# Kernel tuning notes

Measured on AMD Instinct MI355X. Metric: run time of the kernel, lower is better.

Reference implementation:

```python
import jax, jax.numpy as jnp
import numpy as np

N_NODES = 100000
N_EDGES = 1600000
N_GRAPHS = 512
IN_CH = 64
HID = 128
LAT = 64
MAX_NODES = 128
OUT_SIZE = MAX_NODES * (MAX_NODES - 1) // 2  # 8128


def _gcn_conv(x, W, b, src, dst, n):
    """PyG GCNConv: x' = D^-1/2 (A+I) D^-1/2 (x W) + b, degrees include self-loops."""
    h = x @ W  # [N, out]
    deg = jnp.zeros((n,), h.dtype).at[dst].add(1.0) + 1.0  # in-degree + self-loop
    dinv = jax.lax.rsqrt(deg)
    norm = dinv[src] * dinv[dst]  # [E]
    agg = jnp.zeros_like(h).at[dst].add(h[src] * norm[:, None])  # neighbor scatter-add
    agg = agg + h * (dinv * dinv)[:, None]  # self-loop term, norm = 1/deg
    return agg + b


def setup_inputs() -> dict:
    key = jax.random.key(0)
    ks = jax.random.split(key, 20)
    s = 0.02
    inp = {
        "x": jax.random.normal(ks[0], (N_NODES, IN_CH), jnp.float32),
        "edge_index": jax.random.randint(ks[1], (2, N_EDGES), 0, N_NODES),
        "batch": jnp.sort(jax.random.randint(ks[2], (N_NODES,), 0, N_GRAPHS)),
        "eps": jax.random.normal(ks[3], (N_GRAPHS, LAT), jnp.float32),
        # encoder params
        "W1": jax.random.normal(ks[4], (IN_CH, HID), jnp.float32) * s,
        "b1": jnp.zeros((HID,), jnp.float32),
        "W2": jax.random.normal(ks[5], (HID, HID), jnp.float32) * s,
        "b2": jnp.zeros((HID,), jnp.float32),
        "Wmu": jax.random.normal(ks[6], (HID, LAT), jnp.float32) * s,
        "bmu": jnp.zeros((LAT,), jnp.float32),
        "Wlv": jax.random.normal(ks[7], (HID, LAT), jnp.float32) * s,
        "blv": jnp.zeros((LAT,), jnp.float32),
        # decoder MLP params
        "D1": jax.random.normal(ks[8], (LAT, HID), jnp.float32) * s,
        "d1": jnp.zeros((HID,), jnp.float32),
        "D2": jax.random.normal(ks[9], (HID, HID), jnp.float32) * s,
        "d2": jnp.zeros((HID,), jnp.float32),
        "D3": jax.random.normal(ks[10], (HID, OUT_SIZE), jnp.float32) * s,
        "d3": jnp.zeros((OUT_SIZE,), jnp.float32),
    }
    return inp


def reference(x, edge_index, batch, eps, W1, b1, W2, b2, Wmu, bmu, Wlv, blv,
              D1, d1, D2, d2, D3, d3):
    src, dst = edge_index[0], edge_index[1]
    # --- encoder: two GCN layers + ReLU ---
    h = jax.nn.relu(_gcn_conv(x, W1, b1, src, dst, N_NODES))
    h = jax.nn.relu(_gcn_conv(h, W2, b2, src, dst, N_NODES))
    # --- global mean pool by graph id ---
    sums = jax.ops.segment_sum(h, batch, num_segments=N_GRAPHS)
    cnts = jax.ops.segment_sum(jnp.ones((N_NODES,), h.dtype), batch, num_segments=N_GRAPHS)
    h_graph = sums / jnp.maximum(cnts, 1.0)[:, None]  # [G, HID]
    mu = h_graph @ Wmu + bmu
    logvar = h_graph @ Wlv + blv
    # --- reparameterise ---
    z = mu + eps * jnp.exp(0.5 * logvar)  # [G, LAT]
    # --- MLP decoder -> symmetric adjacency ---
    p = jax.nn.relu(z @ D1 + d1)
    p = jax.nn.relu(p @ D2 + d2)
    probs = jax.nn.sigmoid(p @ D3 + d3)  # [G, OUT_SIZE]
    r, c = jnp.triu_indices(MAX_NODES, k=1)
    adj = jnp.zeros((N_GRAPHS, MAX_NODES, MAX_NODES), probs.dtype)
    adj = adj.at[:, r, c].set(probs)
    adj = adj + jnp.swapaxes(adj, 1, 2)
    return adj, mu, logvar
```

## Files before the change

### kernel.cpp

```cpp
#include <hip/hip_runtime.h>
#include <hip/hip_fp16.h>

#define NN 100000
#define NE 1600000
#define NG 512
#define OUTS 8128
#define NB2 196
#define CHUNK 8192
#define NPB 196

typedef short bf16x8 __attribute__((ext_vector_type(8)));
typedef _Float16 f16x8 __attribute__((ext_vector_type(8)));
typedef _Float16 f16x2 __attribute__((ext_vector_type(2)));
typedef float f32x4 __attribute__((ext_vector_type(4)));

__device__ __forceinline__ unsigned pack_bf16x2(float a, float b) {
    unsigned ua = __float_as_uint(a);
    unsigned ub = __float_as_uint(b);
    ua = (ua + 0x7fffu + ((ua >> 16) & 1u)) >> 16;
    ub = (ub + 0x7fffu + ((ub >> 16) & 1u)) >> 16;
    return ua | (ub << 16);
}
__device__ __forceinline__ unsigned short f2bf(float f) {
    unsigned u = __float_as_uint(f);
    u = (u + 0x7fffu + ((u >> 16) & 1u)) >> 16;
    return (unsigned short)u;
}
__device__ __forceinline__ unsigned cvt_pkrtz_u(float a, float b) {
    auto h = __builtin_amdgcn_cvt_pkrtz(a, b);
    union { decltype(h) h2; unsigned u; } c; c.h2 = h; return c.u;
}
__device__ __forceinline__ f16x2 u2h(unsigned u) { union { unsigned u; f16x2 h; } c; c.u = u; return c.h; }

__device__ __forceinline__ unsigned f2fp8(float f) {
    unsigned h = (unsigned)__half_as_ushort(__float2half(f * 0.00390625f));
    return (h + 0x3Fu + ((h >> 7) & 1u)) >> 7;
}
__device__ __forceinline__ unsigned f2fp8s(float f) {
    unsigned h = (unsigned)__half_as_ushort(__float2half(f * 0.00390625f));
    unsigned s = (h >> 8) & 0x80u;
    unsigned mag = h & 0x7fffu;
    return s | ((mag + 0x3Fu + ((mag >> 7) & 1u)) >> 7);
}

#define DECO(W, LO, HI) { LO += u2h(((W) & 0x007f007fu) << 7); HI += u2h(((W) & 0x7f007f00u) >> 1); }
#define DECOS(W, LO, HI) { \
    LO += u2h((((W) & 0x007f007fu) << 7) | (((W) & 0x00800080u) << 8)); \
    HI += u2h((((W) & 0x7f007f00u) >> 1) | ((W) & 0x80008000u)); }

__global__ __launch_bounds__(512) void k_part(const int* __restrict__ src, const int* __restrict__ dst,
        int* __restrict__ tmp, int* __restrict__ scanhist) {
    __shared__ int hist[NB2], cur[NB2], scan[256];
    int p = blockIdx.x, t = threadIdx.x;
    int e0 = p * CHUNK;
    int e1 = min(e0 + CHUNK, NE);
    for (int i = t; i < NB2; i += 512) hist[i] = 0;
    __syncthreads();
    for (int e = e0 + t; e < e1; e += 512)
        atomicAdd(&hist[dst[e] >> 9], 1);
    __syncthreads();
    int h = 0;
    if (t < 256) { h = (t < NB2) ? hist[t] : 0; scan[t] = h; }
    __syncthreads();
    for (int off = 1; off < 256; off <<= 1) {
        int v = (t < 256 && t >= off) ? scan[t - off] : 0;
        __syncthreads();
        if (t < 256) scan[t] += v;
        __syncthreads();
    }
    if (t < NB2) {
        int excl = scan[t] - h;
        cur[t] = excl;
        scanhist[p * (NB2 + 1) + t] = excl;
    }
    if (t == 0) scanhist[p * (NB2 + 1) + NB2] = e1 - e0;
    __syncthreads();
    for (int e = e0 + t; e < e1; e += 512) {
        int d = dst[e];
        int b = d >> 9;
        int r = atomicAdd(&cur[b], 1);
        tmp[e0 + r] = (src[e] << 9) | (d & 511);
    }
}

__global__ __launch_bounds__(256) void k_btotseg(const int* __restrict__ scanhist,
        int* __restrict__ bucketbase, const int* __restrict__ batch, int* __restrict__ seg_end) {
    if (blockIdx.x == 0) {
        __shared__ int sc[256];
        int b = threadIdx.x;
        int tot = 0;
        if (b < NB2) {
            for (int p = 0; p < NPB; ++p)
                tot += scanhist[p * (NB2 + 1) + b + 1] - scanhist[p * (NB2 + 1) + b];
        }
        sc[b] = tot;
        __syncthreads();
        for (int off = 1; off < 256; off <<= 1) {
            int v = (b >= off) ? sc[b - off] : 0;
            __syncthreads();
            sc[b] += v;
            __syncthreads();
        }
        if (b < NB2) bucketbase[b] = sc[b] - tot;
    } else {
        int i = (blockIdx.x - 1) * 256 + threadIdx.x;
        if (i >= NN) return;
        int b = batch[i];
        int bn = (i == NN - 1) ? NG : batch[i + 1];
        for (int g = b; g < bn; ++g) seg_end[g] = i + 1;
        if (i == 0) {
            for (int g = 0; g < b; ++g) seg_end[g] = 0;
        }
    }
}

__global__ __launch_bounds__(1024) void k_fill2(const int* __restrict__ bucketbase,
        const int* __restrict__ scanhist, const int* __restrict__ tmp,
        int* __restrict__ colidx, int* __restrict__ cnti, int* __restrict__ rowptr,
        float* __restrict__ dinv, const float* __restrict__ x, unsigned* __restrict__ u1b) {
    __shared__ int lc[512], rb[512], sc[256];
    __shared__ float ldv[512];
    int b = blockIdx.x, t = threadIdx.x;
    int n0 = b << 9;
    if (t < 512) lc[t] = 0;
    __syncthreads();
    int w = t >> 6, lane = t & 63;
    for (int p = w; p < NPB; p += 16) {
        int s0 = scanhist[p * (NB2 + 1) + b];
        int s1 = scanhist[p * (NB2 + 1) + b + 1];
        int base = p * CHUNK;
        for (int i = s0 + lane; i < s1; i += 64)
            atomicAdd(&lc[tmp[base + i] & 511], 1);
    }
    __syncthreads();
    int v0 = 0, v1 = 0, s = 0;
    if (t < 256) { v0 = lc[2 * t]; v1 = lc[2 * t + 1]; s = v0 + v1; sc[t] = s; }
    __syncthreads();
    for (int off = 1; off < 256; off <<= 1) {
        int xv = (t < 256 && t >= off) ? sc[t - off] : 0;
        __syncthreads();
        if (t < 256) sc[t] += xv;
        __syncthreads();
    }
    if (t < 256) {
        int excl = sc[t] - s;
        int base0 = bucketbase[b];
        rb[2 * t] = base0 + excl;
        rb[2 * t + 1] = base0 + excl + v0;
        float dv0 = rsqrtf((float)v0 + 1.0f);
        float dv1 = rsqrtf((float)v1 + 1.0f);
        ldv[2 * t] = dv0;
        ldv[2 * t + 1] = dv1;
        int node0 = n0 + 2 * t;
        if (node0 < NN) {
            cnti[node0] = v0;
            rowptr[node0] = base0 + excl;
            dinv[node0] = dv0;
        }
        if (node0 + 1 < NN) {
            cnti[node0 + 1] = v1;
            rowptr[node0 + 1] = base0 + excl + v0;
            dinv[node0 + 1] = dv1;
        }
    }
    __syncthreads();
    if (t < 512) lc[t] = 0;
    __syncthreads();
    for (int p = w; p < NPB; p += 16) {
        int s0 = scanhist[p * (NB2 + 1) + b];
        int s1 = scanhist[p * (NB2 + 1) + b + 1];
        int base = p * CHUNK;
        for (int i = s0 + lane; i < s1; i += 64) {
            int v = tmp[base + i];
            int dl = v & 511;
            int pos = atomicAdd(&lc[dl], 1);
            colidx[rb[dl] + pos] = v >> 9;
        }
    }
    for (int i = t; i < 512 * 16; i += 1024) {
        int local = i >> 4, c = i & 15;
        int node = n0 + local;
        if (node >= NN) continue;
        float4 xv = *(const float4*)&x[(long)node * 64 + c * 4];
        float d = ldv[local];
        unsigned o = f2fp8s(xv.x * d) | (f2fp8s(xv.y * d) << 8)
                   | (f2fp8s(xv.z * d) << 16) | (f2fp8s(xv.w * d) << 24);
        u1b[node * 16 + c] = o;
    }
}

__global__ __launch_bounds__(256) void k_wtall(const float* __restrict__ W1,
        const float* __restrict__ W2, const float* __restrict__ D3,
        unsigned short* __restrict__ wt1, unsigned short* __restrict__ wt2,
        unsigned short* __restrict__ wt3t) {
    __shared__ float tile[32][33];
    int blk = blockIdx.x;
    if (blk < 96) {
        int i = blk * 256 + threadIdx.x;
        if (i < 8192) {
            int n = i >> 6, k = i & 63;
            wt1[i] = (unsigned short)__half_as_ushort(__float2half(W1[k * 128 + n]));
        } else {
            int e = i - 8192;
            int n = e >> 7, k = e & 127;
            wt2[e] = f2bf(W2[k * 128 + n]);
        }
    } else {
        int bb = blk - 96;
        int n0 = (bb % 254) * 32, k0 = (bb / 254) * 32;
        for (int i = threadIdx.x; i < 1024; i += 256) {
            int kk = i >> 5, nn = i & 31;
            tile[kk][nn] = D3[(long)(k0 + kk) * OUTS + n0 + nn];
        }
        __syncthreads();
        for (int i = threadIdx.x; i < 1024; i += 256) {
            int nn = i >> 5, kk = i & 31;
            wt3t[(long)(n0 + nn) * 128 + k0 + kk] =
                (unsigned short)__half_as_ushort(__float2half(tile[kk][nn]));
        }
    }
}

__global__ __launch_bounds__(256) void k_gather1(const int* __restrict__ rowptr,
        const int* __restrict__ cnti, const int* __restrict__ colidx,
        const unsigned* __restrict__ u, const float* __restrict__ dinv,
        unsigned* __restrict__ s1) {
    int node = blockIdx.x * 64 + (threadIdx.x >> 2);
    if (node >= NN) return;
    int lane = threadIdx.x & 3;
    const uint4* uf = (const uint4*)u;
    uint4 self = uf[node * 4 + lane];
    f16x2 z = {(_Float16)0.f, (_Float16)0.f};
    f16x2 la0 = z, ha0 = z, la1 = z, ha1 = z, la2 = z, ha2 = z, la3 = z, ha3 = z;
    f16x2 lb0 = z, hb0 = z, lb1 = z, hb1 = z, lb2 = z, hb2 = z, lb3 = z, hb3 = z;
    DECOS(self.x, la0, ha0) DECOS(self.y, la1, ha1) DECOS(self.z, la2, ha2) DECOS(self.w, la3, ha3)
    int n = cnti[node];
    const int* ci = colidx + rowptr[node];
    int j = 0;
    for (; j + 4 <= n; j += 4) {
        uint4 va = uf[ci[j] * 4 + lane];
        uint4 vb = uf[ci[j + 1] * 4 + lane];
        uint4 vc = uf[ci[j + 2] * 4 + lane];
        uint4 vd = uf[ci[j + 3] * 4 + lane];
        DECOS(va.x, la0, ha0) DECOS(va.y, la1, ha1) DECOS(va.z, la2, ha2) DECOS(va.w, la3, ha3)
        DECOS(vb.x, lb0, hb0) DECOS(vb.y, lb1, hb1) DECOS(vb.z, lb2, hb2) DECOS(vb.w, lb3, hb3)
        DECOS(vc.x, la0, ha0) DECOS(vc.y, la1, ha1) DECOS(vc.z, la2, ha2) DECOS(vc.w, la3, ha3)
        DECOS(vd.x, lb0, hb0) DECOS(vd.y, lb1, hb1) DECOS(vd.z, lb2, hb2) DECOS(vd.w, lb3, hb3)
    }
    for (; j < n; ++j) {
        uint4 va = uf[ci[j] * 4 + lane];
        DECOS(va.x, la0, ha0) DECOS(va.y, la1, ha1) DECOS(va.z, la2, ha2) DECOS(va.w, la3, ha3)
    }
    la0 += lb0; ha0 += hb0; la1 += lb1; ha1 += hb1;
    la2 += lb2; ha2 += hb2; la3 += lb3; ha3 += hb3;
    float d = dinv[node] * 256.0f;
    uint4 o1, o2;
    o1.x = cvt_pkrtz_u((float)la0[0] * d, (float)ha0[0] * d);
    o1.y = cvt_pkrtz_u((float)la0[1] * d, (float)ha0[1] * d);
    o1.z = cvt_pkrtz_u((float)la1[0] * d, (float)ha1[0] * d);
    o1.w = cvt_pkrtz_u((float)la1[1] * d, (float)ha1[1] * d);
    o2.x = cvt_pkrtz_u((float)la2[0] * d, (float)ha2[0] * d);
    o2.y = cvt_pkrtz_u((float)la2[1] * d, (float)ha2[1] * d);
    o2.z = cvt_pkrtz_u((float)la3[0] * d, (float)ha3[0] * d);
    o2.w = cvt_pkrtz_u((float)la3[1] * d, (float)ha3[1] * d);
    *(uint4*)&s1[node * 32 + lane * 8] = o1;
    *(uint4*)&s1[node * 32 + lane * 8 + 4] = o2;
}

__global__ __launch_bounds__(256) void k_gather2(const int* __restrict__ rowptr,
        const int* __restrict__ cnti, const int* __restrict__ colidx,
        const unsigned* __restrict__ u, const float* __restrict__ dinv,
        unsigned* __restrict__ s2) {
    int node = blockIdx.x * 32 + (threadIdx.x >> 3);
    int lane = threadIdx.x & 7;
    const uint4* uf = (const uint4*)u;
    uint4 self = uf[node * 8 + lane];
    f16x2 z = {(_Float16)0.f, (_Float16)0.f};
    f16x2 la0 = z, ha0 = z, la1 = z, ha1 = z, la2 = z, ha2 = z, la3 = z, ha3 = z;
    f16x2 lb0 = z, hb0 = z, lb1 = z, hb1 = z, lb2 = z, hb2 = z, lb3 = z, hb3 = z;
    DECO(self.x, la0, ha0) DECO(self.y, la1, ha1) DECO(self.z, la2, ha2) DECO(self.w, la3, ha3)
    int n = cnti[node];
    const int* ci = colidx + rowptr[node];
    int j = 0;
    for (; j + 4 <= n; j += 4) {
        uint4 va = uf[ci[j] * 8 + lane];
        uint4 vb = uf[ci[j + 1] * 8 + lane];
        uint4 vc = uf[ci[j + 2] * 8 + lane];
        uint4 vd = uf[ci[j + 3] * 8 + lane];
        DECO(va.x, la0, ha0) DECO(va.y, la1, ha1) DECO(va.z, la2, ha2) DECO(va.w, la3, ha3)
        DECO(vb.x, lb0, hb0) DECO(vb.y, lb1, hb1) DECO(vb.z, lb2, hb2) DECO(vb.w, lb3, hb3)
        DECO(vc.x, la0, ha0) DECO(vc.y, la1, ha1) DECO(vc.z, la2, ha2) DECO(vc.w, la3, ha3)
        DECO(vd.x, lb0, hb0) DECO(vd.y, lb1, hb1) DECO(vd.z, lb2, hb2) DECO(vd.w, lb3, hb3)
    }
    for (; j < n; ++j) {
        uint4 va = uf[ci[j] * 8 + lane];
        DECO(va.x, la0, ha0) DECO(va.y, la1, ha1) DECO(va.z, la2, ha2) DECO(va.w, la3, ha3)
    }
    la0 += lb0; ha0 += hb0; la1 += lb1; ha1 += hb1;
    la2 += lb2; ha2 += hb2; la3 += lb3; ha3 += hb3;
    float d = dinv[node] * 16.0f;
    uint4 o1, o2;
    o1.x = pack_bf16x2((float)la0[0] * d, (float)ha0[0] * d);
    o1.y = pack_bf16x2((float)la0[1] * d, (float)ha0[1] * d);
    o1.z = pack_bf16x2((float)la1[0] * d, (float)ha1[0] * d);
    o1.w = pack_bf16x2((float)la1[1] * d, (float)ha1[1] * d);
    o2.x = pack_bf16x2((float)la2[0] * d, (float)ha2[0] * d);
    o2.y = pack_bf16x2((float)la2[1] * d, (float)ha2[1] * d);
    o2.z = pack_bf16x2((float)la3[0] * d, (float)ha3[0] * d);
    o2.w = pack_bf16x2((float)la3[1] * d, (float)ha3[1] * d);
    *(uint4*)&s2[node * 64 + lane * 8] = o1;
    *(uint4*)&s2[node * 64 + lane * 8 + 4] = o2;
}

template<int K, int EPI, int AF16>
__global__ __launch_bounds__(256) void k_gemm_mfma(const unsigned short* __restrict__ Ab,
        const unsigned short* __restrict__ wt, const float* __restrict__ dinv,
        const float* __restrict__ bias, void* __restrict__ outp) {
    constexpr int KS = K / 32;
    constexpr int SLOTS = K / 8;
    __shared__ __align__(16) unsigned short wlds[128 * K];
    char* lb = (char*)wlds;
    for (int c = threadIdx.x; c < 128 * SLOTS; c += 256) {
        int n = c / SLOTS, s = c - n * SLOTS;
        *(uint4*)(lb + n * (2 * K) + ((s ^ (n & 7)) << 4)) = *(const uint4*)(wt + c * 8);
    }
    __syncthreads();
    int lane = threadIdx.x & 63;
    int w = threadIdx.x >> 6;
    int r0 = blockIdx.x * 64 + w * 16;
    int arow = r0 + (lane & 15);
    if (arow >= NN) arow = NN - 1;
    bf16x8 af[KS];
    #pragma unroll
    for (int ks = 0; ks < KS; ++ks)
        af[ks] = *(const bf16x8*)&Ab[(long)arow * K + ks * 32 + (lane >> 4) * 8];
    f32x4 acc[8];
    #pragma unroll
    for (int t = 0; t < 8; ++t) acc[t] = (f32x4){0.f, 0.f, 0.f, 0.f};
    #pragma unroll
    for (int ks = 0; ks < KS; ++ks) {
        #pragma unroll
        for (int t = 0; t < 8; ++t) {
            int n = t * 16 + (lane & 15);
            int slot = ks * 4 + (lane >> 4);
            bf16x8 braw = *(const bf16x8*)(lb + n * (2 * K) + ((slot ^ (n & 7)) << 4));
            if constexpr (AF16) {
                union { bf16x8 r; f16x8 h; } ca, cb;
                ca.r = af[ks]; cb.r = braw;
                acc[t] = __builtin_amdgcn_mfma_f32_16x16x32_f16(ca.h, cb.h, acc[t], 0, 0, 0);
            } else {
                acc[t] = __builtin_amdgcn_mfma_f32_16x16x32_bf16(af[ks], braw, acc[t], 0, 0, 0);
            }
        }
    }
    float bv[8];
    #pragma unroll
    for (int t = 0; t < 8; ++t) bv[t] = bias[t * 16 + (lane & 15)];
    #pragma unroll
    for (int r = 0; r < 4; ++r) {
        long row = r0 + (lane >> 4) * 4 + r;
        if (row >= NN) continue;
        float d = dinv[row];
        #pragma unroll
        for (int t = 0; t < 8; ++t) {
            float val = fmaxf(acc[t][r] + bv[t], 0.f);
            int col = t * 16 + (lane & 15);
            if (EPI == 0)
                ((unsigned char*)outp)[row * 128 + col] = (unsigned char)f2fp8(val * (16.0f * d));
            else
                ((unsigned short*)outp)[row * 128 + col] = f2bf(val);
        }
    }
}

__global__ __launch_bounds__(256) void k_pooldec(const unsigned* __restrict__ h,
        const int* __restrict__ seg_end,
        const float* __restrict__ Wmu, const float* __restrict__ bmu,
        const float* __restrict__ Wlv, const float* __restrict__ blv,
        const float* __restrict__ eps,
        const float* __restrict__ D1, const float* __restrict__ d1,
        const float* __restrict__ D2, const float* __restrict__ d2,
        float* __restrict__ mu_o, float* __restrict__ lv_o,
        unsigned short* __restrict__ p2out) {
    __shared__ float part[3][128];
    __shared__ float row[128], mlv[128], zr[64], p1[128];
    int g = blockIdx.x;
    int w = threadIdx.x >> 6, t64 = threadIdx.x & 63;
    int s = (g == 0) ? 0 : seg_end[g - 1];
    int e = seg_end[g];
    float a0 = 0.f, a1 = 0.f;
    for (int i = s + w; i < e; i += 4) {
        unsigned u = h[(long)i * 64 + t64];
        a0 += __uint_as_float(u << 16);
        a1 += __uint_as_float(u & 0xffff0000u);
    }
    if (w) { part[w - 1][t64 * 2] = a0; part[w - 1][t64 * 2 + 1] = a1; }
    __syncthreads();
    if (w == 0) {
        a0 += part[0][t64 * 2] + part[1][t64 * 2] + part[2][t64 * 2];
        a1 += part[0][t64 * 2 + 1] + part[1][t64 * 2 + 1] + part[2][t64 * 2 + 1];
        float inv = (e > s) ? 1.0f / (float)(e - s) : 0.f;
        row[t64 * 2] = a0 * inv;
        row[t64 * 2 + 1] = a1 * inv;
    }
    __syncthreads();
    int t = threadIdx.x;
    if (t < 64) {
        float acc = bmu[t];
        for (int k = 0; k < 128; ++k) acc += row[k] * Wmu[k * 64 + t];
        mlv[t] = acc;
    } else if (t < 128) {
        int t2 = t - 64;
        float acc = blv[t2];
        for (int k = 0; k < 128; ++k) acc += row[k] * Wlv[k * 64 + t2];
        mlv[64 + t2] = acc;
    }
    __syncthreads();
    if (t < 64) {
        float mu = mlv[t], lv = mlv[64 + t];
        mu_o[g * 64 + t] = mu;
        lv_o[g * 64 + t] = lv;
        zr[t] = mu + eps[g * 64 + t] * expf(0.5f * lv);
    }
    __syncthreads();
    if (t < 128) {
        float acc = d1[t];
        for (int k = 0; k < 64; ++k) acc += zr[k] * D1[k * 128 + t];
        p1[t] = fmaxf(acc, 0.f);
    }
    __syncthreads();
    if (t < 128) {
        float acc = d2[t];
        for (int k = 0; k < 128; ++k) acc += p1[k] * D2[k * 128 + t];
        p2out[g * 128 + t] = (unsigned short)__half_as_ushort(__float2half(fmaxf(acc, 0.f)));
    }
}

__global__ __launch_bounds__(256) void k_dec3m(const unsigned short* __restrict__ Ab,
        const unsigned short* __restrict__ Wt, const float* __restrict__ b,
        float* __restrict__ out) {
    int lane = threadIdx.x & 63;
    int w = threadIdx.x >> 6;
    int r0 = blockIdx.x * 64 + w * 16;
    int c0 = blockIdx.y * 64;
    int arow = r0 + (lane & 15);
    f16x8 af[4];
    #pragma unroll
    for (int ks = 0; ks < 4; ++ks) {
        union { bf16x8 r; f16x8 h; } ca;
        ca.r = *(const bf16x8*)&Ab[arow * 128 + ks * 32 + (lane >> 4) * 8];
        af[ks] = ca.h;
    }
    f32x4 acc[4];
    #pragma unroll
    for (int nt = 0; nt < 4; ++nt) acc[nt] = (f32x4){0.f, 0.f, 0.f, 0.f};
    #pragma unroll
    for (int nt = 0; nt < 4; ++nt) {
        long n = c0 + nt * 16 + (lane & 15);
        #pragma unroll
        for (int ks = 0; ks < 4; ++ks) {
            union { bf16x8 r; f16x8 h; } cb;
            cb.r = *(const bf16x8*)&Wt[n * 128 + ks * 32 + (lane >> 4) * 8];
            acc[nt] = __builtin_amdgcn_mfma_f32_16x16x32_f16(af[ks], cb.h, acc[nt], 0, 0, 0);
        }
    }
    #pragma unroll
    for (int nt = 0; nt < 4; ++nt) {
        int col = c0 + nt * 16 + (lane & 15);
        float bias = b[col];
        #pragma unroll
        for (int r = 0; r < 4; ++r) {
            int row = r0 + (lane >> 4) * 4 + r;
            float v = acc[nt][r] + bias;
            out[(long)row * OUTS + col] = 1.f / (1.f + expf(-v));
        }
    }
}

__global__ __launch_bounds__(256) void k_adj(const float* __restrict__ probs, float* __restrict__ adj) {
    int t = blockIdx.x * 256 + threadIdx.x;
    int g = t >> 12;
    int rem = t & 4095;
    int r = rem >> 5;
    int c0 = (rem & 31) * 4;
    const float* pg = &probs[g * OUTS];
    float4 o;
    float* op = (float*)&o;
    #pragma unroll
    for (int j = 0; j < 4; ++j) {
        int c = c0 + j;
        if (c == r) { op[j] = 0.f; continue; }
        int a = c < r ? c : r;
        int b = c < r ? r : c;
        int k = a * (255 - a) / 2 + (b - a - 1);
        op[j] = pg[k];
    }
    *(float4*)&adj[(long)t * 4] = o;
}

extern "C" void kernel_launch(void* const* d_in, const int* in_sizes, int n_in,
                              void* d_out, int out_size, void* d_ws, size_t ws_size,
                              hipStream_t stream) {
    const float* x   = (const float*)d_in[0];
    const int*   ei  = (const int*)d_in[1];
    const int* batch = (const int*)d_in[2];
    const float* eps = (const float*)d_in[3];
    const float* W1  = (const float*)d_in[4];
    const float* b1  = (const float*)d_in[5];
    const float* W2  = (const float*)d_in[6];
    const float* b2  = (const float*)d_in[7];
    const float* Wmu = (const float*)d_in[8];
    const float* bmu = (const float*)d_in[9];
    const float* Wlv = (const float*)d_in[10];
    const float* blv = (const float*)d_in[11];
    const float* D1  = (const float*)d_in[12];
    const float* d1  = (const float*)d_in[13];
    const float* D2  = (const float*)d_in[14];
    const float* d2  = (const float*)d_in[15];
    const float* D3  = (const float*)d_in[16];
    const float* d3  = (const float*)d_in[17];

    const int* esrc = ei;
    const int* edst = ei + NE;

    float* out  = (float*)d_out;
    float* mu_o = out + 8388608;
    float* lv_o = mu_o + 32768;

    int*   colidx   = (int*)out;
    int*   cnti     = colidx + 1600000;
    int*   rowptr   = cnti + 100000;
    int*   seg_end  = rowptr + 100000;
    float* dinv     = (float*)(seg_end + 512);
    int*   scanhist = (int*)(dinv + 100000);
    int*   bucketbase = scanhist + 38612;
    unsigned short* wt3t = (unsigned short*)(bucketbase + 256);

    float* ws = (float*)d_ws;
    unsigned* u1b = (unsigned*)ws;
    unsigned* s1u = (unsigned*)(ws + 3200000);
    unsigned char* u2b = (unsigned char*)(ws + 6400000);
    unsigned* s2u = (unsigned*)(ws + 9600000);
    unsigned* h2b = (unsigned*)(ws + 16000000);
    unsigned short* wt1 = (unsigned short*)(ws + 22400000);
    unsigned short* wt2 = wt1 + 8192;
    int* tmp = (int*)(ws + 22420000);
    unsigned short* p2b = (unsigned short*)ws;
    float* probs = ws + 65536;

    k_part<<<NPB, 512, 0, stream>>>(esrc, edst, tmp, scanhist);
    k_btotseg<<<392, 256, 0, stream>>>(scanhist, bucketbase, batch, seg_end);
    k_fill2<<<NB2, 1024, 0, stream>>>(bucketbase, scanhist, tmp, colidx, cnti, rowptr,
                                      dinv, x, u1b);

    k_wtall<<<1112, 256, 0, stream>>>(W1, W2, D3, wt1, wt2, wt3t);

    k_gather1<<<1563, 256, 0, stream>>>(rowptr, cnti, colidx, u1b, dinv, s1u);
    k_gemm_mfma<64, 0, 1><<<1563, 256, 0, stream>>>((const unsigned short*)s1u, wt1, dinv, b1, u2b);

    k_gather2<<<3125, 256, 0, stream>>>(rowptr, cnti, colidx, (const unsigned*)u2b, dinv, s2u);
    k_gemm_mfma<128, 1, 0><<<1563, 256, 0, stream>>>((const unsigned short*)s2u, wt2, dinv, b2, h2b);

    k_pooldec<<<NG, 256, 0, stream>>>(h2b, seg_end, Wmu, bmu, Wlv, blv, eps,
                                      D1, d1, D2, d2, mu_o, lv_o, p2b);

    dim3 g3(8, 127);
    k_dec3m<<<g3, 256, 0, stream>>>(p2b, wt3t, d3, probs);
    k_adj<<<8192, 256, 0, stream>>>(probs, out);
}
```

Before: 205.7 us.

## Fuse neighbor gather with MFMA GEMM per GCN layer and merge weight prep

Each GCN layer's CSR gather-aggregate is merged into the MFMA GEMM kernel, so the gathered features are built directly in the MFMA A-fragment register layout and the intermediate s1/s2 buffers are never written to or read back from global memory. The weight transpose/convert kernel is folded into the edge-partition kernel as extra blocks, saving a launch. The cost is lower gather parallelism: each 16-lane group now gathers narrow uint2 slices per node instead of wide uint4 rows with more nodes per block. Register pressure also rises, which can reduce occupancy for the irregular gather.

```diff
diff --git a/kernel.cpp b/kernel.cpp
--- a/kernel.cpp
+++ b/kernel.cpp
@@ -49,9 +49,42 @@
     HI += u2h((((W) & 0x7f007f00u) >> 1) | ((W) & 0x80008000u)); }
 
 __global__ __launch_bounds__(512) void k_part(const int* __restrict__ src, const int* __restrict__ dst,
-        int* __restrict__ tmp, int* __restrict__ scanhist) {
+        int* __restrict__ tmp, int* __restrict__ scanhist,
+        const float* __restrict__ W1, const float* __restrict__ W2, const float* __restrict__ D3,
+        unsigned short* __restrict__ wt1, unsigned short* __restrict__ wt2,
+        unsigned short* __restrict__ wt3t) {
+    int t = threadIdx.x;
+    if (blockIdx.x >= NPB) {
+        int blk2 = blockIdx.x - NPB;
+        if (blk2 < 48) {
+            int i = blk2 * 512 + t;
+            if (i < 8192) {
+                int n = i >> 6, k = i & 63;
+                wt1[i] = (unsigned short)__half_as_ushort(__float2half(W1[k * 128 + n]));
+            } else {
+                int e = i - 8192;
+                int n = e >> 7, k = e & 127;
+                wt2[e] = f2bf(W2[k * 128 + n]);
+            }
+        } else {
+            __shared__ float tile[32][33];
+            int bb = blk2 - 48;
+            int n0 = (bb % 254) * 32, k0 = (bb / 254) * 32;
+            for (int i = t; i < 1024; i += 512) {
+                int kk = i >> 5, nn = i & 31;
+                tile[kk][nn] = D3[(long)(k0 + kk) * OUTS + n0 + nn];
+            }
+            __syncthreads();
+            for (int i = t; i < 1024; i += 512) {
+                int nn = i >> 5, kk = i & 31;
+                wt3t[(long)(n0 + nn) * 128 + k0 + kk] =
+                    (unsigned short)__half_as_ushort(__float2half(tile[kk][nn]));
+            }
+        }
+        return;
+    }
     __shared__ int hist[NB2], cur[NB2], scan[256];
-    int p = blockIdx.x, t = threadIdx.x;
+    int p = blockIdx.x;
     int e0 = p * CHUNK;
     int e1 = min(e0 + CHUNK, NE);
     for (int i = t; i < NB2; i += 512) hist[i] = 0;
@@ -189,168 +222,85 @@
     }
 }
 
-__global__ __launch_bounds__(256) void k_wtall(const float* __restrict__ W1,
-        const float* __restrict__ W2, const float* __restrict__ D3,
-        unsigned short* __restrict__ wt1, unsigned short* __restrict__ wt2,
-        unsigned short* __restrict__ wt3t) {
-    __shared__ float tile[32][33];
-    int blk = blockIdx.x;
-    if (blk < 96) {
-        int i = blk * 256 + threadIdx.x;
-        if (i < 8192) {
-            int n = i >> 6, k = i & 63;
-            wt1[i] = (unsigned short)__half_as_ushort(__float2half(W1[k * 128 + n]));
-        } else {
-            int e = i - 8192;
-            int n = e >> 7, k = e & 127;
-            wt2[e] = f2bf(W2[k * 128 + n]);
-        }
-    } else {
-        int bb = blk - 96;
-        int n0 = (bb % 254) * 32, k0 = (bb / 254) * 32;
-        for (int i = threadIdx.x; i < 1024; i += 256) {
-            int kk = i >> 5, nn = i & 31;
-            tile[kk][nn] = D3[(long)(k0 + kk) * OUTS + n0 + nn];
-        }
-        __syncthreads();
-        for (int i = threadIdx.x; i < 1024; i += 256) {
-            int nn = i >> 5, kk = i & 31;
-            wt3t[(long)(n0 + nn) * 128 + k0 + kk] =
-                (unsigned short)__half_as_ushort(__float2half(tile[kk][nn]));
-        }
-    }
-}
-
-__global__ __launch_bounds__(256) void k_gather1(const int* __restrict__ rowptr,
+__global__ __launch_bounds__(256) void k_gconv1(const int* __restrict__ rowptr,
         const int* __restrict__ cnti, const int* __restrict__ colidx,
         const unsigned* __restrict__ u, const float* __restrict__ dinv,
-        unsigned* __restrict__ s1) {
-    int node = blockIdx.x * 64 + (threadIdx.x >> 2);
-    if (node >= NN) return;
-    int lane = threadIdx.x & 3;
-    const uint4* uf = (const uint4*)u;
-    uint4 self = uf[node * 4 + lane];
-    f16x2 z = {(_Float16)0.f, (_Float16)0.f};
-    f16x2 la0 = z, ha0 = z, la1 = z, ha1 = z, la2 = z, ha2 = z, la3 = z, ha3 = z;
-    f16x2 lb0 = z, hb0 = z, lb1 = z, hb1 = z, lb2 = z, hb2 = z, lb3 = z, hb3 = z;
-    DECOS(self.x, la0, ha0) DECOS(self.y, la1, ha1) DECOS(self.z, la2, ha2) DECOS(self.w, la3, ha3)
-    int n = cnti[node];
-    const int* ci = colidx + rowptr[node];
-    int j = 0;
-    for (; j + 4 <= n; j += 4) {
-        uint4 va = uf[ci[j] * 4 + lane];
-        uint4 vb = uf[ci[j + 1] * 4 + lane];
-        uint4 vc = uf[ci[j + 2] * 4 + lane];
-        uint4 vd = uf[ci[j + 3] * 4 + lane];
-        DECOS(va.x, la0, ha0) DECOS(va.y, la1, ha1) DECOS(va.z, la2, ha2) DECOS(va.w, la3, ha3)
-        DECOS(vb.x, lb0, hb0) DECOS(vb.y, lb1, hb1) DECOS(vb.z, lb2, hb2) DECOS(vb.w, lb3, hb3)
-        DECOS(vc.x, la0, ha0) DECOS(vc.y, la1, ha1) DECOS(vc.z, la2, ha2) DECOS(vc.w, la3, ha3)
-        DECOS(vd.x, lb0, hb0) DECOS(vd.y, lb1, hb1) DECOS(vd.z, lb2, hb2) DECOS(vd.w, lb3, hb3)
-    }
-    for (; j < n; ++j) {
-        uint4 va = uf[ci[j] * 4 + lane];
-        DECOS(va.x, la0, ha0) DECOS(va.y, la1, ha1) DECOS(va.z, la2, ha2) DECOS(va.w, la3, ha3)
-    }
-    la0 += lb0; ha0 += hb0; la1 += lb1; ha1 += hb1;
-    la2 += lb2; ha2 += hb2; la3 += lb3; ha3 += hb3;
-    float d = dinv[node] * 256.0f;
-    uint4 o1, o2;
-    o1.x = cvt_pkrtz_u((float)la0[0] * d, (float)ha0[0] * d);
-    o1.y = cvt_pkrtz_u((float)la0[1] * d, (float)ha0[1] * d);
-    o1.z = cvt_pkrtz_u((float)la1[0] * d, (float)ha1[0] * d);
-    o1.w = cvt_pkrtz_u((float)la1[1] * d, (float)ha1[1] * d);
-    o2.x = cvt_pkrtz_u((float)la2[0] * d, (float)ha2[0] * d);
-    o2.y = cvt_pkrtz_u((float)la2[1] * d, (float)ha2[1] * d);
-    o2.z = cvt_pkrtz_u((float)la3[0] * d, (float)ha3[0] * d);
-    o2.w = cvt_pkrtz_u((float)la3[1] * d, (float)ha3[1] * d);
-    *(uint4*)&s1[node * 32 + lane * 8] = o1;
-    *(uint4*)&s1[node * 32 + lane * 8 + 4] = o2;
-}
-
-__global__ __launch_bounds__(256) void k_gather2(const int* __restrict__ rowptr,
-        const int* __restrict__ cnti, const int* __restrict__ colidx,
-        const unsigned* __restrict__ u, const float* __restrict__ dinv,
-        unsigned* __restrict__ s2) {
-    int node = blockIdx.x * 32 + (threadIdx.x >> 3);
-    int lane = threadIdx.x & 7;
-    const uint4* uf = (const uint4*)u;
-    uint4 self = uf[node * 8 + lane];
-    f16x2 z = {(_Float16)0.f, (_Float16)0.f};
-    f16x2 la0 = z, ha0 = z, la1 = z, ha1 = z, la2 = z, ha2 = z, la3 = z, ha3 = z;
-    f16x2 lb0 = z, hb0 = z, lb1 = z, hb1 = z, lb2 = z, hb2 = z, lb3 = z, hb3 = z;
-    DECO(self.x, la0, ha0) DECO(self.y, la1, ha1) DECO(self.z, la2, ha2) DECO(self.w, la3, ha3)
-    int n = cnti[node];
-    const int* ci = colidx + rowptr[node];
-    int j = 0;
-    for (; j + 4 <= n; j += 4) {
-        uint4 va = uf[ci[j] * 8 + lane];
-        uint4 vb = uf[ci[j + 1] * 8 + lane];
-        uint4 vc = uf[ci[j + 2] * 8 + lane];
-        uint4 vd = uf[ci[j + 3] * 8 + lane];
-        DECO(va.x, la0, ha0) DECO(va.y, la1, ha1) DECO(va.z, la2, ha2) DECO(va.w, la3, ha3)
-        DECO(vb.x, lb0, hb0) DECO(vb.y, lb1, hb1) DECO(vb.z, lb2, hb2) DECO(vb.w, lb3, hb3)
-        DECO(vc.x, la0, ha0) DECO(vc.y, la1, ha1) DECO(vc.z, la2, ha2) DECO(vc.w, la3, ha3)
-        DECO(vd.x, lb0, hb0) DECO(vd.y, lb1, hb1) DECO(vd.z, lb2, hb2) DECO(vd.w, lb3, hb3)
-    }
-    for (; j < n; ++j) {
-        uint4 va = uf[ci[j] * 8 + lane];
-        DECO(va.x, la0, ha0) DECO(va.y, la1, ha1) DECO(va.z, la2, ha2) DECO(va.w, la3, ha3)
-    }
-    la0 += lb0; ha0 += hb0; la1 += lb1; ha1 += hb1;
-    la2 += lb2; ha2 += hb2; la3 += lb3; ha3 += hb3;
-    float d = dinv[node] * 16.0f;
-    uint4 o1, o2;
-    o1.x = pack_bf16x2((float)la0[0] * d, (float)ha0[0] * d);
-    o1.y = pack_bf16x2((float)la0[1] * d, (float)ha0[1] * d);
-    o1.z = pack_bf16x2((float)la1[0] * d, (float)ha1[0] * d);
-    o1.w = pack_bf16x2((float)la1[1] * d, (float)ha1[1] * d);
-    o2.x = pack_bf16x2((float)la2[0] * d, (float)ha2[0] * d);
-    o2.y = pack_bf16x2((float)la2[1] * d, (float)ha2[1] * d);
-    o2.z = pack_bf16x2((float)la3[0] * d, (float)ha3[0] * d);
-    o2.w = pack_bf16x2((float)la3[1] * d, (float)ha3[1] * d);
-    *(uint4*)&s2[node * 64 + lane * 8] = o1;
-    *(uint4*)&s2[node * 64 + lane * 8 + 4] = o2;
-}
-
-template<int K, int EPI, int AF16>
-__global__ __launch_bounds__(256) void k_gemm_mfma(const unsigned short* __restrict__ Ab,
-        const unsigned short* __restrict__ wt, const float* __restrict__ dinv,
-        const float* __restrict__ bias, void* __restrict__ outp) {
-    constexpr int KS = K / 32;
-    constexpr int SLOTS = K / 8;
+        const unsigned short* __restrict__ wt, const float* __restrict__ bias,
+        unsigned char* __restrict__ outp) {
+    constexpr int K = 64, SLOTS = 8;
     __shared__ __align__(16) unsigned short wlds[128 * K];
     char* lb = (char*)wlds;
     for (int c = threadIdx.x; c < 128 * SLOTS; c += 256) {
         int n = c / SLOTS, s = c - n * SLOTS;
         *(uint4*)(lb + n * (2 * K) + ((s ^ (n & 7)) << 4)) = *(const uint4*)(wt + c * 8);
     }
-    __syncthreads();
     int lane = threadIdx.x & 63;
     int w = threadIdx.x >> 6;
     int r0 = blockIdx.x * 64 + w * 16;
-    int arow = r0 + (lane & 15);
-    if (arow >= NN) arow = NN - 1;
-    bf16x8 af[KS];
-    #pragma unroll
-    for (int ks = 0; ks < KS; ++ks)
-        af[ks] = *(const bf16x8*)&Ab[(long)arow * K + ks * 32 + (lane >> 4) * 8];
+    int node = r0 + (lane & 15);
+    if (node >= NN) node = NN - 1;
+    int kg = lane >> 4;
+    const uint2* uf = (const uint2*)u;
+    f16x2 z = {(_Float16)0.f, (_Float16)0.f};
+    f16x2 A0l = z, A0h = z, A1l = z, A1h = z;
+    f16x2 B0l = z, B0h = z, B1l = z, B1h = z;
+    f16x2 A0l2 = z, A0h2 = z, A1l2 = z, A1h2 = z;
+    f16x2 B0l2 = z, B0h2 = z, B1l2 = z, B1h2 = z;
+    {
+        uint2 s0 = uf[node * 8 + kg];
+        uint2 s1v = uf[node * 8 + 4 + kg];
+        DECOS(s0.x, A0l, A0h) DECOS(s0.y, A1l, A1h)
+        DECOS(s1v.x, B0l, B0h) DECOS(s1v.y, B1l, B1h)
+    }
+    int n = cnti[node];
+    const int* ci = colidx + rowptr[node];
+    int j = 0;
+    for (; j + 2 <= n; j += 2) {
+        int sa = ci[j], sb = ci[j + 1];
+        uint2 a0 = uf[sa * 8 + kg];
+        uint2 a1 = uf[sa * 8 + 4 + kg];
+        uint2 b0 = uf[sb * 8 + kg];
+        uint2 b1 = uf[sb * 8 + 4 + kg];
+        DECOS(a0.x, A0l, A0h) DECOS(a0.y, A1l, A1h)
+        DECOS(a1.x, B0l, B0h) DECOS(a1.y, B1l, B1h)
+        DECOS(b0.x, A0l2, A0h2) DECOS(b0.y, A1l2, A1h2)
+        DECOS(b1.x, B0l2, B0h2) DECOS(b1.y, B1l2, B1h2)
+    }
+    if (j < n) {
+        int sa = ci[j];
+        uint2 a0 = uf[sa * 8 + kg];
+        uint2 a1 = uf[sa * 8 + 4 + kg];
+        DECOS(a0.x, A0l, A0h) DECOS(a0.y, A1l, A1h)
+        DECOS(a1.x, B0l, B0h) DECOS(a1.y, B1l, B1h)
+    }
+    A0l += A0l2; A0h += A0h2; A1l += A1l2; A1h += A1h2;
+    B0l += B0l2; B0h += B0h2; B1l += B1l2; B1h += B1h2;
+    float d = dinv[node] * 256.0f;
+    union { uint4 u4; f16x8 h; } fa0, fa1;
+    fa0.u4.x = cvt_pkrtz_u((float)A0l[0] * d, (float)A0h[0] * d);
+    fa0.u4.y = cvt_pkrtz_u((float)A0l[1] * d, (float)A0h[1] * d);
+    fa0.u4.z = cvt_pkrtz_u((float)A1l[0] * d, (float)A1h[0] * d);
+    fa0.u4.w = cvt_pkrtz_u((float)A1l[1] * d, (float)A1h[1] * d);
+    fa1.u4.x = cvt_pkrtz_u((float)B0l[0] * d, (float)B0h[0] * d);
+    fa1.u4.y = cvt_pkrtz_u((float)B0l[1] * d, (float)B0h[1] * d);
+    fa1.u4.z = cvt_pkrtz_u((float)B1l[0] * d, (float)B1h[0] * d);
+    fa1.u4.w = cvt_pkrtz_u((float)B1l[1] * d, (float)B1h[1] * d);
+    __syncthreads();
     f32x4 acc[8];
     #pragma unroll
     for (int t = 0; t < 8; ++t) acc[t] = (f32x4){0.f, 0.f, 0.f, 0.f};
     #pragma unroll
-    for (int ks = 0; ks < KS; ++ks) {
-        #pragma unroll
-        for (int t = 0; t < 8; ++t) {
-            int n = t * 16 + (lane & 15);
-            int slot = ks * 4 + (lane >> 4);
-            bf16x8 braw = *(const bf16x8*)(lb + n * (2 * K) + ((slot ^ (n & 7)) << 4));
-            if constexpr (AF16) {
-                union { bf16x8 r; f16x8 h; } ca, cb;
-                ca.r = af[ks]; cb.r = braw;
-                acc[t] = __builtin_amdgcn_mfma_f32_16x16x32_f16(ca.h, cb.h, acc[t], 0, 0, 0);
-            } else {
-                acc[t] = __builtin_amdgcn_mfma_f32_16x16x32_bf16(af[ks], braw, acc[t], 0, 0, 0);
-            }
+    for (int t = 0; t < 8; ++t) {
+        int nn = t * 16 + (lane & 15);
+        {
+            union { bf16x8 r; f16x8 h; } cb;
+            cb.r = *(const bf16x8*)(lb + nn * (2 * K) + (((0 * 4 + kg) ^ (nn & 7)) << 4));
+            acc[t] = __builtin_amdgcn_mfma_f32_16x16x32_f16(fa0.h, cb.h, acc[t], 0, 0, 0);
+        }
+        {
+            union { bf16x8 r; f16x8 h; } cb;
+            cb.r = *(const bf16x8*)(lb + nn * (2 * K) + (((1 * 4 + kg) ^ (nn & 7)) << 4));
+            acc[t] = __builtin_amdgcn_mfma_f32_16x16x32_f16(fa1.h, cb.h, acc[t], 0, 0, 0);
         }
     }
     float bv[8];
@@ -360,15 +310,114 @@
     for (int r = 0; r < 4; ++r) {
         long row = r0 + (lane >> 4) * 4 + r;
         if (row >= NN) continue;
-        float d = dinv[row];
+        float dd = dinv[row];
         #pragma unroll
         for (int t = 0; t < 8; ++t) {
             float val = fmaxf(acc[t][r] + bv[t], 0.f);
-            int col = t * 16 + (lane & 15);
-            if (EPI == 0)
-                ((unsigned char*)outp)[row * 128 + col] = (unsigned char)f2fp8(val * (16.0f * d));
-            else
-                ((unsigned short*)outp)[row * 128 + col] = f2bf(val);
+            outp[row * 128 + t * 16 + (lane & 15)] = (unsigned char)f2fp8(val * (16.0f * dd));
+        }
+    }
+}
+
+__global__ __launch_bounds__(256) void k_gconv2(const int* __restrict__ rowptr,
+        const int* __restrict__ cnti, const int* __restrict__ colidx,
+        const unsigned* __restrict__ u, const float* __restrict__ dinv,
+        const unsigned short* __restrict__ wt, const float* __restrict__ bias,
+        unsigned short* __restrict__ outp) {
+    constexpr int K = 128, SLOTS = 16;
+    __shared__ __align__(16) unsigned short wlds[128 * K];
+    char* lb = (char*)wlds;
+    for (int c = threadIdx.x; c < 128 * SLOTS; c += 256) {
+        int n = c / SLOTS, s = c - n * SLOTS;
+        *(uint4*)(lb + n * (2 * K) + ((s ^ (n & 7)) << 4)) = *(const uint4*)(wt + c * 8);
+    }
+    int lane = threadIdx.x & 63;
+    int w = threadIdx.x >> 6;
+    int r0 = blockIdx.x * 64 + w * 16;
+    int node = r0 + (lane & 15);
+    if (node >= NN) node = NN - 1;
+    int kg = lane >> 4;
+    const uint2* uf = (const uint2*)u;
+    f16x2 z = {(_Float16)0.f, (_Float16)0.f};
+    f16x2 L0[4], H0[4], L1[4], H1[4];
+    f16x2 L0s[4], H0s[4], L1s[4], H1s[4];
+    #pragma unroll
+    for (int ks = 0; ks < 4; ++ks) { L0[ks]=z; H0[ks]=z; L1[ks]=z; H1[ks]=z;
+                                     L0s[ks]=z; H0s[ks]=z; L1s[ks]=z; H1s[ks]=z; }
+    #pragma unroll
+    for (int ks = 0; ks < 4; ++ks) {
+        uint2 sv = uf[node * 16 + ks * 4 + kg];
+        DECO(sv.x, L0[ks], H0[ks]) DECO(sv.y, L1[ks], H1[ks])
+    }
+    int n = cnti[node];
+    const int* ci = colidx + rowptr[node];
+    int j = 0;
+    for (; j + 2 <= n; j += 2) {
+        int sa = ci[j], sb = ci[j + 1];
+        uint2 a0 = uf[sa * 16 + kg];
+        uint2 a1 = uf[sa * 16 + 4 + kg];
+        uint2 a2 = uf[sa * 16 + 8 + kg];
+        uint2 a3 = uf[sa * 16 + 12 + kg];
+        uint2 b0 = uf[sb * 16 + kg];
+        uint2 b1 = uf[sb * 16 + 4 + kg];
+        uint2 b2 = uf[sb * 16 + 8 + kg];
+        uint2 b3 = uf[sb * 16 + 12 + kg];
+        DECO(a0.x, L0[0], H0[0]) DECO(a0.y, L1[0], H1[0])
+        DECO(a1.x, L0[1], H0[1]) DECO(a1.y, L1[1], H1[1])
+        DECO(a2.x, L0[2], H0[2]) DECO(a2.y, L1[2], H1[2])
+        DECO(a3.x, L0[3], H0[3]) DECO(a3.y, L1[3], H1[3])
+        DECO(b0.x, L0s[0], H0s[0]) DECO(b0.y, L1s[0], H1s[0])
+        DECO(b1.x, L0s[1], H0s[1]) DECO(b1.y, L1s[1], H1s[1])
+        DECO(b2.x, L0s[2], H0s[2]) DECO(b2.y, L1s[2], H1s[2])
+        DECO(b3.x, L0s[3], H0s[3]) DECO(b3.y, L1s[3], H1s[3])
+    }
+    if (j < n) {
+        int sa = ci[j];
+        #pragma unroll
+        for (int ks = 0; ks < 4; ++ks) {
+            uint2 av = uf[sa * 16 + ks * 4 + kg];
+            DECO(av.x, L0[ks], H0[ks]) DECO(av.y, L1[ks], H1[ks])
+        }
+    }
+    #pragma unroll
+    for (int ks = 0; ks < 4; ++ks) {
+        L0[ks] += L0s[ks]; H0[ks] += H0s[ks];
+        L1[ks] += L1s[ks]; H1[ks] += H1s[ks];
+    }
+    float d = dinv[node] * 16.0f;
+    union { uint4 u4; bf16x8 r; } fa[4];
+    #pragma unroll
+    for (int ks = 0; ks < 4; ++ks) {
+        fa[ks].u4.x = pack_bf16x2((float)L0[ks][0] * d, (float)H0[ks][0] * d);
+        fa[ks].u4.y = pack_bf16x2((float)L0[ks][1] * d, (float)H0[ks][1] * d);
+        fa[ks].u4.z = pack_bf16x2((float)L1[ks][0] * d, (float)H1[ks][0] * d);
+        fa[ks].u4.w = pack_bf16x2((float)L1[ks][1] * d, (float)H1[ks][1] * d);
+    }
+    __syncthreads();
+    f32x4 acc[8];
+    #pragma unroll
+    for (int t = 0; t < 8; ++t) acc[t] = (f32x4){0.f, 0.f, 0.f, 0.f};
+    #pragma unroll
+    for (int ks = 0; ks < 4; ++ks) {
+        #pragma unroll
+        for (int t = 0; t < 8; ++t) {
+            int nn = t * 16 + (lane & 15);
+            int slot = ks * 4 + kg;
+            bf16x8 braw = *(const bf16x8*)(lb + nn * (2 * K) + ((slot ^ (nn & 7)) << 4));
+            acc[t] = __builtin_amdgcn_mfma_f32_16x16x32_bf16(fa[ks].r, braw, acc[t], 0, 0, 0);
+        }
+    }
+    float bv[8];
+    #pragma unroll
+    for (int t = 0; t < 8; ++t) bv[t] = bias[t * 16 + (lane & 15)];
+    #pragma unroll
+    for (int r = 0; r < 4; ++r) {
+        long row = r0 + (lane >> 4) * 4 + r;
+        if (row >= NN) continue;
+        #pragma unroll
+        for (int t = 0; t < 8; ++t) {
+            float val = fmaxf(acc[t][r] + bv[t], 0.f);
+            outp[row * 128 + t * 16 + (lane & 15)] = f2bf(val);
         }
     }
 }
@@ -538,9 +587,7 @@
 
     float* ws = (float*)d_ws;
     unsigned* u1b = (unsigned*)ws;
-    unsigned* s1u = (unsigned*)(ws + 3200000);
     unsigned char* u2b = (unsigned char*)(ws + 6400000);
-    unsigned* s2u = (unsigned*)(ws + 9600000);
     unsigned* h2b = (unsigned*)(ws + 16000000);
     unsigned short* wt1 = (unsigned short*)(ws + 22400000);
     unsigned short* wt2 = wt1 + 8192;
@@ -548,18 +595,16 @@
     unsigned short* p2b = (unsigned short*)ws;
     float* probs = ws + 65536;
 
-    k_part<<<NPB, 512, 0, stream>>>(esrc, edst, tmp, scanhist);
+    k_part<<<NPB + 48 + 1016, 512, 0, stream>>>(esrc, edst, tmp, scanhist,
+                                                W1, W2, D3, wt1, wt2, wt3t);
     k_btotseg<<<392, 256, 0, stream>>>(scanhist, bucketbase, batch, seg_end);
     k_fill2<<<NB2, 1024, 0, stream>>>(bucketbase, scanhist, tmp, colidx, cnti, rowptr,
                                       dinv, x, u1b);
 
-    k_wtall<<<1112, 256, 0, stream>>>(W1, W2, D3, wt1, wt2, wt3t);
-
-    k_gather1<<<1563, 256, 0, stream>>>(rowptr, cnti, colidx, u1b, dinv, s1u);
-    k_gemm_mfma<64, 0, 1><<<1563, 256, 0, stream>>>((const unsigned short*)s1u, wt1, dinv, b1, u2b);
-
-    k_gather2<<<3125, 256, 0, stream>>>(rowptr, cnti, colidx, (const unsigned*)u2b, dinv, s2u);
-    k_gemm_mfma<128, 1, 0><<<1563, 256, 0, stream>>>((const unsigned short*)s2u, wt2, dinv, b2, h2b);
+    k_gconv1<<<1563, 256, 0, stream>>>(rowptr, cnti, colidx, u1b, dinv, wt1, b1, u2b);
+
+    k_gconv2<<<1563, 256, 0, stream>>>(rowptr, cnti, colidx, (const unsigned*)u2b, dinv,
+                                       wt2, b2, (unsigned short*)h2b);
 
     k_pooldec<<<NG, 256, 0, stream>>>(h2b, seg_end, Wmu, bmu, Wlv, blv, eps,
                                       D1, d1, D2, d2, mu_o, lv_o, p2b);
```

Measured after the change: 230.5 us. 12.0% more time.
